# Kernel tuning notes

Hardware: AMD Instinct MI355X
Metric: run time of the kernel (lower is better)

## Reference

```python
import jax, jax.numpy as jnp
import numpy as np
from jax import lax

B, C_IN, C_OUT, H, W, K, MID = 16, 256, 256, 64, 64, 3, 64
BN_EPS = 1e-5


def setup_inputs() -> dict:
    key = jax.random.key(0)
    ks = jax.random.split(key, 16)
    inp = {
        'x': jax.random.normal(ks[0], (B, C_IN, H, W), dtype=jnp.float32),
        # 4 kernel banks: (4, c2, c1//g, k, k)
        'weight': jax.random.normal(ks[1], (4, C_OUT, C_IN, K, K), dtype=jnp.float32) * 0.05,
        'gamma': jnp.ones((C_OUT,), jnp.float32),
        'beta': jnp.zeros((C_OUT,), jnp.float32),
    }
    # four attention branches: Linear(c, mid, bias=False) -> ReLU -> Linear(mid, 4, bias=True)
    names = ['s', 'c', 'f', 'w']
    for i, n in enumerate(names):
        inp[f'fc_{n}_w1'] = jax.random.normal(ks[2 + 3 * i], (MID, C_IN), dtype=jnp.float32) * 0.05
        inp[f'fc_{n}_w2'] = jax.random.normal(ks[3 + 3 * i], (4, MID), dtype=jnp.float32) * 0.05
        inp[f'fc_{n}_b2'] = jax.random.normal(ks[4 + 3 * i], (4,), dtype=jnp.float32) * 0.05
    return inp


def _branch(pooled, w1, w2, b2):
    # pooled: [B, C]; w1: [MID, C]; w2: [4, MID]
    h = jax.nn.relu(pooled @ w1.T)
    return jax.nn.softmax(h @ w2.T + b2, axis=1)  # [B, 4]


def reference(x, weight, gamma, beta,
              fc_s_w1, fc_s_w2, fc_s_b2,
              fc_c_w1, fc_c_w2, fc_c_b2,
              fc_f_w1, fc_f_w2, fc_f_b2,
              fc_w_w1, fc_w_w2, fc_w_b2):
    b = x.shape[0]
    pooled = jnp.mean(x, axis=(2, 3))  # GAP -> [B, C]
    alpha = (_branch(pooled, fc_s_w1, fc_s_w2, fc_s_b2)
             * _branch(pooled, fc_c_w1, fc_c_w2, fc_c_b2)
             * _branch(pooled, fc_f_w1, fc_f_w2, fc_f_b2)
             * _branch(pooled, fc_w_w1, fc_w_w2, fc_w_b2))  # [B, 4]
    # per-sample dynamic kernels: [B, out_c, in_c, k, k]
    dyn_w = jnp.einsum('bn,noikl->boikl', alpha, weight)

    def conv_one(xi, wi):
        # xi: [C, H, W]; wi: [out_c, in_c, k, k]
        return lax.conv_general_dilated(
            xi[None], wi, window_strides=(1, 1), padding='SAME',
            dimension_numbers=('NCHW', 'OIHW', 'NCHW'))[0]

    out = jax.vmap(conv_one)(x, dyn_w)  # [B, out_c, H, W]

    # BatchNorm2d (training-mode batch statistics)
    mean = jnp.mean(out, axis=(0, 2, 3))
    var = jnp.var(out, axis=(0, 2, 3))
    out = (out - mean[None, :, None, None]) * jax.lax.rsqrt(var + BN_EPS)[None, :, None, None]
    return out * gamma[None, :, None, None] + beta[None, :, None, None]
```

## Files before the change

### kernel.cpp

```cpp
#include <hip/hip_runtime.h>
#include <math.h>

#define BB 16
#define CIN 256
#define COUT 256
#define HH 64
#define WW 64
#define NBANK_STRIDE 589824

typedef short bf16x8 __attribute__((ext_vector_type(8)));
typedef float f32x4 __attribute__((ext_vector_type(4)));

#define WS_XT_OFF 32768
#define WS_DW_OFF 33587200
#define WS_NEED   52461568ULL

static __device__ __forceinline__ short f2bf(float f) {
    union { float f; unsigned u; } v; v.f = f;
    unsigned r = v.u + 0x7FFF + ((v.u >> 16) & 1);
    return (short)(r >> 16);
}

struct AttnParams {
    const float* w1[4];
    const float* w2[4];
    const float* b2[4];
};

__global__ __launch_bounds__(256) void zero_kernel(float* __restrict__ ws) {
    ws[blockIdx.x * 256 + threadIdx.x] = 0.f;
}

__global__ __launch_bounds__(256) void xpose_kernel(const float* __restrict__ x,
                                                    short* __restrict__ xT,
                                                    float* __restrict__ pooled) {
    const int ci0 = blockIdx.x * 32;
    const int h = blockIdx.y;
    const int b = blockIdx.z;
    const int t = threadIdx.x;
    __shared__ __align__(16) short tile[64][40];
    {
        const int ci = t >> 3;
        const int l = t & 7;
        const float4* src = (const float4*)(x + ((size_t)(b * 256 + ci0 + ci)) * 4096 + h * 64);
        float4 v1 = src[l * 2];
        float4 v2 = src[l * 2 + 1];
        tile[l * 8 + 0][ci] = f2bf(v1.x);
        tile[l * 8 + 1][ci] = f2bf(v1.y);
        tile[l * 8 + 2][ci] = f2bf(v1.z);
        tile[l * 8 + 3][ci] = f2bf(v1.w);
        tile[l * 8 + 4][ci] = f2bf(v2.x);
        tile[l * 8 + 5][ci] = f2bf(v2.y);
        tile[l * 8 + 6][ci] = f2bf(v2.z);
        tile[l * 8 + 7][ci] = f2bf(v2.w);
        float s = v1.x + v1.y + v1.z + v1.w + v2.x + v2.y + v2.z + v2.w;
        s += __shfl_xor(s, 1, 64);
        s += __shfl_xor(s, 2, 64);
        s += __shfl_xor(s, 4, 64);
        if (l == 0) atomicAdd(&pooled[b * 256 + ci0 + ci], s);
    }
    __syncthreads();
    {
        const int w = t >> 2;
        const int s = t & 3;
        bf16x8 val = *(const bf16x8*)&tile[w][s * 8];
        *(bf16x8*)&xT[((size_t)b * 4096 + h * 64 + w) * 256 + ci0 + s * 8] = val;
    }
}

__global__ __launch_bounds__(256) void attn_kernel(AttnParams p, float* __restrict__ ws_f) {
    const int b = blockIdx.x;
    const int t = threadIdx.x;
    const int wv = t >> 6;
    const int lane = t & 63;
    __shared__ float ps[256];
    __shared__ float hs[4][64];
    __shared__ float lg[4][4];
    __shared__ float sm[4][4];
    ws_f[4096 + b * 256 + t] = 0.f;
    ps[t] = ws_f[b * 256 + t] * (1.0f / 4096.0f);
    __syncthreads();
    {
        const float4* w1v = (const float4*)(p.w1[wv] + lane * 256);
        float h = 0.f;
#pragma unroll 8
        for (int i = 0; i < 64; ++i) {
            float4 w4 = w1v[i];
            h += w4.x * ps[i * 4 + 0] + w4.y * ps[i * 4 + 1] +
                 w4.z * ps[i * 4 + 2] + w4.w * ps[i * 4 + 3];
        }
        hs[wv][lane] = fmaxf(h, 0.f);
    }
    __syncthreads();
    if (t < 16) {
        const int n = t >> 2, j = t & 3;
        const float* w2 = p.w2[n];
        float l = p.b2[n][j];
        for (int m = 0; m < 64; ++m) l += w2[j * 64 + m] * hs[n][m];
        lg[n][j] = l;
    }
    __syncthreads();
    if (t < 4) {
        const int n = t;
        float mx = fmaxf(fmaxf(lg[n][0], lg[n][1]), fmaxf(lg[n][2], lg[n][3]));
        float e0 = expf(lg[n][0] - mx), e1 = expf(lg[n][1] - mx);
        float e2 = expf(lg[n][2] - mx), e3 = expf(lg[n][3] - mx);
        float inv = 1.f / (e0 + e1 + e2 + e3);
        sm[n][0] = e0 * inv; sm[n][1] = e1 * inv; sm[n][2] = e2 * inv; sm[n][3] = e3 * inv;
    }
    __syncthreads();
    if (t < 4) ws_f[b * 256 + t] = sm[0][t] * sm[1][t] * sm[2][t] * sm[3][t];
}

__global__ __launch_bounds__(256) void dynw_kernel(const float* __restrict__ wt,
                                                   const float* __restrict__ ws_f,
                                                   short* __restrict__ dynwF) {
    const int co = blockIdx.x;
    const int ci = threadIdx.x;
    const int cotile = co >> 4;
    const int mh = co & 15;
    const int cc = ci >> 5;
    const int q = (ci >> 3) & 3;
    const int j = ci & 7;
    const int lane = q * 16 + mh;
    float w[4][9];
#pragma unroll
    for (int n = 0; n < 4; ++n) {
        const size_t base = ((size_t)(n * 256 + co) * 256 + ci) * 9;
#pragma unroll
        for (int k = 0; k < 9; ++k) w[n][k] = wt[base + k];
    }
    for (int b = 0; b < BB; ++b) {
        const float a0 = ws_f[b * 256 + 0];
        const float a1 = ws_f[b * 256 + 1];
        const float a2 = ws_f[b * 256 + 2];
        const float a3 = ws_f[b * 256 + 3];
#pragma unroll
        for (int k = 0; k < 9; ++k) {
            float v = a0 * w[0][k] + a1 * w[1][k] + a2 * w[2][k] + a3 * w[3][k];
            dynwF[(((((size_t)(b * 9 + k) * 16 + cotile) * 8 + cc) * 64 + lane) << 3) + j] = f2bf(v);
        }
    }
}

__global__ __launch_bounds__(256, 2) void conv_mfma_kernel(const short* __restrict__ xT,
                                                           const short* __restrict__ dynwF,
                                                           float* __restrict__ out,
                                                           float* __restrict__ bn_part) {
    const int id = blockIdx.x;
    const int xcd = id & 7;
    const int wi = id >> 3;
    const int b = xcd + ((wi >> 5) << 3);
    const int rem = wi & 31;
    const int mt = rem >> 4;
    const int nt = rem & 15;

    const int t = threadIdx.x;
    const int lane = t & 63;
    const int wv = t >> 6;
    const int wx = wv & 1;
    const int wy = wv >> 1;
    const int mh = lane & 15;
    const int q = lane >> 4;
    const int r0 = nt * 4;
    const int co0 = mt * 128;

    __shared__ __align__(16) short xs[396 * 64];
    __shared__ __align__(16) short As[2][4096];
    __shared__ float red[128][2][2];

    f32x4 acc[4][8];
#pragma unroll
    for (int i = 0; i < 4; ++i)
#pragma unroll
        for (int j = 0; j < 8; ++j) acc[i][j] = (f32x4){0.f, 0.f, 0.f, 0.f};

    const size_t a_b9 = (size_t)b * 9;
    const int a_ct = mt * 8 + (t >> 5);
    const int a_port16 = (t & 31) * 16;
    const int a_dst = (t >> 5) * 512 + a_port16;
    const int a_rd0 = (wy * 4) * 512 + lane * 8;

    const bf16x8 zero8 = {0, 0, 0, 0, 0, 0, 0, 0};

    for (int cc = 0; cc < 8; ++cc) {
        const int ci0 = cc * 32;
        __syncthreads();
        const short* asrc0 = dynwF + ((((a_b9 + 0) * 16 + a_ct) * 8 + cc) << 9) + a_port16;
        bf16x8 pa0 = *(const bf16x8*)(asrc0);
        bf16x8 pa1 = *(const bf16x8*)(asrc0 + 8);
#pragma unroll
        for (int i = 0; i < 7; ++i) {
            int idx = t + 256 * i;
            if (idx < 1584) {
                int p = idx >> 2;
                int sub = idx & 3;
                int lr = p / 66;
                int lc = p - lr * 66;
                int r = r0 - 1 + lr;
                int c = lc - 1;
                bf16x8 v = zero8;
                if ((unsigned)r < 64u && (unsigned)c < 64u)
                    v = *(const bf16x8*)&xT[((size_t)b * 4096 + r * 64 + c) * 256 + ci0 + sub * 8];
                *(bf16x8*)&xs[(p << 6) + ((sub ^ (p & 7)) << 3)] = v;
            }
        }
        *(bf16x8*)&As[0][a_dst] = pa0;
        *(bf16x8*)&As[0][a_dst + 8] = pa1;
        __syncthreads();
#pragma unroll
        for (int khw = 0; khw < 9; ++khw) {
            const int kh = khw / 3;
            const int kw = khw - kh * 3;
            bf16x8 na0, na1;
            if (khw < 8) {
                const short* s = dynwF + ((((a_b9 + khw + 1) * 16 + a_ct) * 8 + cc) << 9) + a_port16;
                na0 = *(const bf16x8*)(s);
                na1 = *(const bf16x8*)(s + 8);
            }
            bf16x8 bfr[8];
#pragma unroll
            for (int ni = 0; ni < 8; ++ni) {
                const int row_l = wx * 2 + (ni >> 2) + kh;
                const int col_l = (ni & 3) * 16 + kw + mh;
                const int pp = row_l * 66 + col_l;
                bfr[ni] = *(const bf16x8*)&xs[(pp << 6) + ((q ^ (pp & 7)) << 3)];
            }
#pragma unroll
            for (int mi = 0; mi < 4; ++mi) {
                bf16x8 af = *(const bf16x8*)&As[khw & 1][a_rd0 + mi * 512];
#pragma unroll
                for (int ni = 0; ni < 8; ++ni)
                    acc[mi][ni] = __builtin_amdgcn_mfma_f32_16x16x32_bf16(af, bfr[ni], acc[mi][ni], 0, 0, 0);
            }
            if (khw < 8) {
                *(bf16x8*)&As[(khw + 1) & 1][a_dst] = na0;
                *(bf16x8*)&As[(khw + 1) & 1][a_dst + 8] = na1;
                __syncthreads();
            }
        }
    }

    float s16[4][4], q16[4][4];
#pragma unroll
    for (int mi = 0; mi < 4; ++mi)
#pragma unroll
        for (int reg = 0; reg < 4; ++reg) { s16[mi][reg] = 0.f; q16[mi][reg] = 0.f; }

#pragma unroll
    for (int mi = 0; mi < 4; ++mi) {
#pragma unroll
        for (int ni = 0; ni < 8; ++ni) {
            const int pix = wx * 128 + ni * 16 + mh;
            const int h = r0 + (pix >> 6);
            const int w = pix & 63;
#pragma unroll
            for (int reg = 0; reg < 4; ++reg) {
                const int co = co0 + wy * 64 + mi * 16 + q * 4 + reg;
                const float e = acc[mi][ni][reg];
                out[(((size_t)b * 256 + co) << 12) + (h << 6) + w] = e;
                s16[mi][reg] += e;
                q16[mi][reg] += e * e;
            }
        }
    }
#pragma unroll
    for (int mi = 0; mi < 4; ++mi)
#pragma unroll
        for (int reg = 0; reg < 4; ++reg) {
            float s = s16[mi][reg], sq = q16[mi][reg];
            s += __shfl_xor(s, 1, 64);  sq += __shfl_xor(sq, 1, 64);
            s += __shfl_xor(s, 2, 64);  sq += __shfl_xor(sq, 2, 64);
            s += __shfl_xor(s, 4, 64);  sq += __shfl_xor(sq, 4, 64);
            s += __shfl_xor(s, 8, 64);  sq += __shfl_xor(sq, 8, 64);
            if (mh == 0) {
                const int co_l = wy * 64 + mi * 16 + q * 4 + reg;
                red[co_l][0][wx] = s;
                red[co_l][1][wx] = sq;
            }
        }
    __syncthreads();
    {
        const int co_l = t >> 1;
        const int st = t & 1;
        float v = red[co_l][st][0] + red[co_l][st][1];
        atomicAdd(&bn_part[(st * 256 + co0 + co_l) * 8 + (nt & 7)], v);
    }
}

__global__ __launch_bounds__(256) void bn_finalize_kernel(const float* __restrict__ bn_part,
                                                          const float* __restrict__ gamma,
                                                          const float* __restrict__ beta,
                                                          float* __restrict__ scale,
                                                          float* __restrict__ shift) {
    const int co = threadIdx.x;
    float S = 0.f, Q = 0.f;
#pragma unroll
    for (int s = 0; s < 8; ++s) {
        S += bn_part[(co) * 8 + s];
        Q += bn_part[(256 + co) * 8 + s];
    }
    const float mean = S * (1.f / 65536.f);
    const float var = Q * (1.f / 65536.f) - mean * mean;
    const float inv = rsqrtf(var + 1e-5f);
    const float sc = gamma[co] * inv;
    scale[co] = sc;
    shift[co] = beta[co] - mean * sc;
}

__global__ __launch_bounds__(256) void bn_apply_kernel(float* __restrict__ out,
                                                       const float* __restrict__ scale,
                                                       const float* __restrict__ shift) {
    const int gid = blockIdx.x * 256 + threadIdx.x;
    const int c = (gid >> 10) & 255;
    float4* p = (float4*)out;
    float4 v = p[gid];
    const float sc = scale[c], sh = shift[c];
    v.x = v.x * sc + sh;
    v.y = v.y * sc + sh;
    v.z = v.z * sc + sh;
    v.w = v.w * sc + sh;
    p[gid] = v;
}

__global__ __launch_bounds__(256) void gap_kernel(const float* __restrict__ x,
                                                  float* __restrict__ pooled) {
    const int plane = blockIdx.x;
    const float4* p = (const float4*)(x + (size_t)plane * 4096);
    const int t = threadIdx.x;
    float s = 0.f;
#pragma unroll
    for (int i = 0; i < 4; ++i) {
        float4 v = p[t + 256 * i];
        s += v.x + v.y + v.z + v.w;
    }
#pragma unroll
    for (int off = 32; off > 0; off >>= 1) s += __shfl_down(s, off, 64);
    __shared__ float red[4];
    if ((t & 63) == 0) red[t >> 6] = s;
    __syncthreads();
    if (t == 0) pooled[plane] = (red[0] + red[1] + red[2] + red[3]) * (1.0f / 4096.0f);
}

__global__ __launch_bounds__(64) void attn64_kernel(const float* __restrict__ pooled,
                                                    AttnParams p,
                                                    float* __restrict__ alpha) {
    const int b = blockIdx.x;
    const int t = threadIdx.x;
    __shared__ float ps[256];
    __shared__ float hs[64];
    __shared__ float lg[4];
    __shared__ float prod[4];
#pragma unroll
    for (int i = 0; i < 4; ++i) ps[t + 64 * i] = pooled[b * 256 + t + 64 * i];
    if (t < 4) prod[t] = 1.f;
    __syncthreads();
    for (int n = 0; n < 4; ++n) {
        const float* w1 = p.w1[n];
        float h = 0.f;
        for (int c = 0; c < 256; ++c) h += w1[t * 256 + c] * ps[c];
        hs[t] = fmaxf(h, 0.f);
        __syncthreads();
        if (t < 4) {
            const float* w2 = p.w2[n];
            float l = p.b2[n][t];
            for (int m = 0; m < 64; ++m) l += w2[t * 64 + m] * hs[m];
            lg[t] = l;
        }
        __syncthreads();
        if (t == 0) {
            float mx = fmaxf(fmaxf(lg[0], lg[1]), fmaxf(lg[2], lg[3]));
            float e0 = expf(lg[0] - mx), e1 = expf(lg[1] - mx);
            float e2 = expf(lg[2] - mx), e3 = expf(lg[3] - mx);
            float inv = 1.f / (e0 + e1 + e2 + e3);
            prod[0] *= e0 * inv; prod[1] *= e1 * inv;
            prod[2] *= e2 * inv; prod[3] *= e3 * inv;
        }
        __syncthreads();
    }
    if (t < 4) alpha[b * 4 + t] = prod[t];
}

__global__ __launch_bounds__(256) void conv_fp32_kernel(const float* __restrict__ x,
                                                        const float* __restrict__ wt,
                                                        const float* __restrict__ alpha,
                                                        float* __restrict__ out) {
    const int h = blockIdx.x;
    const int cot = blockIdx.y;
    const int b = blockIdx.z;
    const int t = threadIdx.x;
    const int tx = t & 15;
    const int ty = t >> 4;
    const int co0 = cot * 64;
    __shared__ __align__(16) float xsf[32][68];
    __shared__ __align__(16) float wshf[3][32][68];
    const float a0 = alpha[b * 4 + 0], a1 = alpha[b * 4 + 1];
    const float a2 = alpha[b * 4 + 2], a3 = alpha[b * 4 + 3];
    float acc[4][4];
#pragma unroll
    for (int i = 0; i < 4; ++i)
#pragma unroll
        for (int j = 0; j < 4; ++j) acc[i][j] = 0.f;
    const size_t xbase = (size_t)b * CIN * 4096;
    for (int kh = 0; kh < 3; ++kh) {
        const int r = h + kh - 1;
        if (r < 0 || r >= HH) continue;
        for (int chunk = 0; chunk < 8; ++chunk) {
            const int ci0 = chunk * 32;
            __syncthreads();
#pragma unroll
            for (int i = 0; i < 8; ++i) {
                int flat = t + 256 * i;
                int ci = flat >> 6;
                int w = flat & 63;
                xsf[ci][1 + w] = x[xbase + (size_t)(ci0 + ci) * 4096 + r * 64 + w];
            }
            if (t < 32) { xsf[t][0] = 0.f; xsf[t][65] = 0.f; xsf[t][66] = 0.f; xsf[t][67] = 0.f; }
#pragma unroll
            for (int j = 0; j < 24; ++j) {
                int e = t + 256 * j;
                int co = e / 96;
                int rem = e - co * 96;
                int ci = rem / 3;
                int kw = rem - ci * 3;
                size_t g = (((size_t)(co0 + co) * 256 + (ci0 + ci)) * 3 + kh) * 3 + kw;
                wshf[kw][ci][co] = a0 * wt[g] + a1 * wt[g + NBANK_STRIDE] +
                                   a2 * wt[g + 2 * NBANK_STRIDE] + a3 * wt[g + 3 * NBANK_STRIDE];
            }
            __syncthreads();
            for (int ci = 0; ci < 32; ++ci) {
                float4 w0 = *(const float4*)&wshf[0][ci][tx * 4];
                float4 w1v = *(const float4*)&wshf[1][ci][tx * 4];
                float4 w2v = *(const float4*)&wshf[2][ci][tx * 4];
                float4 xa = *(const float4*)&xsf[ci][ty * 4];
                float4 xb = *(const float4*)&xsf[ci][ty * 4 + 4];
                float v[8] = {xa.x, xa.y, xa.z, xa.w, xb.x, xb.y, xb.z, xb.w};
                float aw[3][4] = {{w0.x, w0.y, w0.z, w0.w},
                                  {w1v.x, w1v.y, w1v.z, w1v.w},
                                  {w2v.x, w2v.y, w2v.z, w2v.w}};
#pragma unroll
                for (int kw = 0; kw < 3; ++kw)
#pragma unroll
                    for (int i = 0; i < 4; ++i)
#pragma unroll
                        for (int j = 0; j < 4; ++j)
                            acc[i][j] += aw[kw][i] * v[j + kw];
            }
        }
    }
    size_t obase = (((size_t)b * COUT + co0 + tx * 4) * 64 + h) * 64 + ty * 4;
#pragma unroll
    for (int i = 0; i < 4; ++i) {
        float4 o = {acc[i][0], acc[i][1], acc[i][2], acc[i][3]};
        *(float4*)&out[obase + (size_t)i * 4096] = o;
    }
}

__global__ __launch_bounds__(256) void bn_stats_kernel(const float* __restrict__ out,
                                                       const float* __restrict__ gamma,
                                                       const float* __restrict__ beta,
                                                       float* __restrict__ scale,
                                                       float* __restrict__ shift) {
    const int co = blockIdx.x;
    const int t = threadIdx.x;
    float s = 0.f, sq = 0.f;
    for (int b = 0; b < BB; ++b) {
        const float4* p = (const float4*)(out + ((size_t)b * 256 + co) * 4096);
#pragma unroll
        for (int i = 0; i < 4; ++i) {
            float4 v = p[t + 256 * i];
            s += v.x + v.y + v.z + v.w;
            sq += v.x * v.x + v.y * v.y + v.z * v.z + v.w * v.w;
        }
    }
#pragma unroll
    for (int off = 32; off > 0; off >>= 1) {
        s += __shfl_down(s, off, 64);
        sq += __shfl_down(sq, off, 64);
    }
    __shared__ float rs[4], rq[4];
    if ((t & 63) == 0) { rs[t >> 6] = s; rq[t >> 6] = sq; }
    __syncthreads();
    if (t == 0) {
        float S = rs[0] + rs[1] + rs[2] + rs[3];
        float Q = rq[0] + rq[1] + rq[2] + rq[3];
        float mean = S * (1.f / 65536.f);
        float var = Q * (1.f / 65536.f) - mean * mean;
        float inv = rsqrtf(var + 1e-5f);
        float sc = gamma[co] * inv;
        scale[co] = sc;
        shift[co] = beta[co] - mean * sc;
    }
}

extern "C" void kernel_launch(void* const* d_in, const int* in_sizes, int n_in,
                              void* d_out, int out_size, void* d_ws, size_t ws_size,
                              hipStream_t stream) {
    (void)in_sizes; (void)n_in; (void)out_size;
    const float* x = (const float*)d_in[0];
    const float* wt = (const float*)d_in[1];
    const float* gamma = (const float*)d_in[2];
    const float* beta = (const float*)d_in[3];
    AttnParams ap;
    for (int n = 0; n < 4; ++n) {
        ap.w1[n] = (const float*)d_in[4 + 3 * n];
        ap.w2[n] = (const float*)d_in[5 + 3 * n];
        ap.b2[n] = (const float*)d_in[6 + 3 * n];
    }
    float* ws_f = (float*)d_ws;
    float* out = (float*)d_out;

    if (ws_size >= WS_NEED) {
        short* xT = (short*)((char*)d_ws + WS_XT_OFF);
        short* dynwF = (short*)((char*)d_ws + WS_DW_OFF);
        float* bn_part = ws_f + 4096;
        float* scale = ws_f;
        float* shift = ws_f + 256;

        zero_kernel<<<16, 256, 0, stream>>>(ws_f);
        xpose_kernel<<<dim3(8, 64, 16), 256, 0, stream>>>(x, xT, ws_f);
        attn_kernel<<<16, 256, 0, stream>>>(ap, ws_f);
        dynw_kernel<<<256, 256, 0, stream>>>(wt, ws_f, dynwF);
        conv_mfma_kernel<<<512, 256, 0, stream>>>(xT, dynwF, out, bn_part);
        bn_finalize_kernel<<<1, 256, 0, stream>>>(bn_part, gamma, beta, scale, shift);
        bn_apply_kernel<<<16384, 256, 0, stream>>>(out, scale, shift);
    } else {
        float* pooled = ws_f;
        float* alpha = ws_f + 4096;
        float* scale = ws_f + 4160;
        float* shift = ws_f + 4416;
        gap_kernel<<<4096, 256, 0, stream>>>(x, pooled);
        attn64_kernel<<<16, 64, 0, stream>>>(pooled, ap, alpha);
        conv_fp32_kernel<<<dim3(64, 4, 16), 256, 0, stream>>>(x, wt, alpha, out);
        bn_stats_kernel<<<256, 256, 0, stream>>>(out, gamma, beta, scale, shift);
        bn_apply_kernel<<<16384, 256, 0, stream>>>(out, scale, shift);
    }
}
```

Before: 274.3 us.

## Fuse BN finalize into apply, coalesce dynw stores, batch xpose rows, memset zeroing

Folds the BN finalize kernel into the apply kernel so each block recomputes its channel's scale and shift from the partial sums, removing one launch. The dynamic-weight kernel now stages bf16 values in shared memory and writes 16-byte vectors instead of scattered 2-byte stores. The transpose kernel handles four rows per block, accumulating the pooled sum locally so it issues fewer atomics, and the zero kernel is replaced with hipMemsetAsync. The cost is redundant per-block BN stat reads and extra barriers in the transpose and dynw kernels.

```diff
diff --git a/kernel.cpp b/kernel.cpp
--- a/kernel.cpp
+++ b/kernel.cpp
@@ -27,45 +27,46 @@
     const float* b2[4];
 };
 
-__global__ __launch_bounds__(256) void zero_kernel(float* __restrict__ ws) {
-    ws[blockIdx.x * 256 + threadIdx.x] = 0.f;
-}
-
 __global__ __launch_bounds__(256) void xpose_kernel(const float* __restrict__ x,
                                                     short* __restrict__ xT,
                                                     float* __restrict__ pooled) {
     const int ci0 = blockIdx.x * 32;
-    const int h = blockIdx.y;
+    const int h0 = blockIdx.y * 4;
     const int b = blockIdx.z;
     const int t = threadIdx.x;
     __shared__ __align__(16) short tile[64][40];
-    {
-        const int ci = t >> 3;
-        const int l = t & 7;
-        const float4* src = (const float4*)(x + ((size_t)(b * 256 + ci0 + ci)) * 4096 + h * 64);
-        float4 v1 = src[l * 2];
-        float4 v2 = src[l * 2 + 1];
-        tile[l * 8 + 0][ci] = f2bf(v1.x);
-        tile[l * 8 + 1][ci] = f2bf(v1.y);
-        tile[l * 8 + 2][ci] = f2bf(v1.z);
-        tile[l * 8 + 3][ci] = f2bf(v1.w);
-        tile[l * 8 + 4][ci] = f2bf(v2.x);
-        tile[l * 8 + 5][ci] = f2bf(v2.y);
-        tile[l * 8 + 6][ci] = f2bf(v2.z);
-        tile[l * 8 + 7][ci] = f2bf(v2.w);
-        float s = v1.x + v1.y + v1.z + v1.w + v2.x + v2.y + v2.z + v2.w;
-        s += __shfl_xor(s, 1, 64);
-        s += __shfl_xor(s, 2, 64);
-        s += __shfl_xor(s, 4, 64);
-        if (l == 0) atomicAdd(&pooled[b * 256 + ci0 + ci], s);
-    }
-    __syncthreads();
-    {
-        const int w = t >> 2;
-        const int s = t & 3;
-        bf16x8 val = *(const bf16x8*)&tile[w][s * 8];
-        *(bf16x8*)&xT[((size_t)b * 4096 + h * 64 + w) * 256 + ci0 + s * 8] = val;
-    }
+    const int ci = t >> 3;
+    const int l = t & 7;
+    const int w = t >> 2;
+    const int s4 = t & 3;
+    float sacc = 0.f;
+    for (int hh = 0; hh < 4; ++hh) {
+        const int h = h0 + hh;
+        __syncthreads();
+        {
+            const float4* src = (const float4*)(x + ((size_t)(b * 256 + ci0 + ci)) * 4096 + h * 64);
+            float4 v1 = src[l * 2];
+            float4 v2 = src[l * 2 + 1];
+            tile[l * 8 + 0][ci] = f2bf(v1.x);
+            tile[l * 8 + 1][ci] = f2bf(v1.y);
+            tile[l * 8 + 2][ci] = f2bf(v1.z);
+            tile[l * 8 + 3][ci] = f2bf(v1.w);
+            tile[l * 8 + 4][ci] = f2bf(v2.x);
+            tile[l * 8 + 5][ci] = f2bf(v2.y);
+            tile[l * 8 + 6][ci] = f2bf(v2.z);
+            tile[l * 8 + 7][ci] = f2bf(v2.w);
+            sacc += v1.x + v1.y + v1.z + v1.w + v2.x + v2.y + v2.z + v2.w;
+        }
+        __syncthreads();
+        {
+            bf16x8 val = *(const bf16x8*)&tile[w][s4 * 8];
+            *(bf16x8*)&xT[((size_t)b * 4096 + h * 64 + w) * 256 + ci0 + s4 * 8] = val;
+        }
+    }
+    sacc += __shfl_xor(sacc, 1, 64);
+    sacc += __shfl_xor(sacc, 2, 64);
+    sacc += __shfl_xor(sacc, 4, 64);
+    if (l == 0) atomicAdd(&pooled[b * 256 + ci0 + ci], sacc);
 }
 
 __global__ __launch_bounds__(256) void attn_kernel(AttnParams p, float* __restrict__ ws_f) {
@@ -119,10 +120,7 @@
     const int ci = threadIdx.x;
     const int cotile = co >> 4;
     const int mh = co & 15;
-    const int cc = ci >> 5;
-    const int q = (ci >> 3) & 3;
-    const int j = ci & 7;
-    const int lane = q * 16 + mh;
+    __shared__ __align__(16) short st[9][272];
     float w[4][9];
 #pragma unroll
     for (int n = 0; n < 4; ++n) {
@@ -136,10 +134,22 @@
         const float a2 = ws_f[b * 256 + 2];
         const float a3 = ws_f[b * 256 + 3];
 #pragma unroll
-        for (int k = 0; k < 9; ++k) {
-            float v = a0 * w[0][k] + a1 * w[1][k] + a2 * w[2][k] + a3 * w[3][k];
-            dynwF[(((((size_t)(b * 9 + k) * 16 + cotile) * 8 + cc) * 64 + lane) << 3) + j] = f2bf(v);
-        }
+        for (int k = 0; k < 9; ++k)
+            st[k][ci] = f2bf(a0 * w[0][k] + a1 * w[1][k] + a2 * w[2][k] + a3 * w[3][k]);
+        __syncthreads();
+#pragma unroll
+        for (int i = 0; i < 2; ++i) {
+            const int task = ci + 256 * i;
+            if (task < 288) {
+                const int k = task >> 5;
+                const int c5 = task & 31;
+                const int cc = c5 >> 2;
+                const int q = c5 & 3;
+                bf16x8 v = *(const bf16x8*)&st[k][cc * 32 + q * 8];
+                *(bf16x8*)&dynwF[((size_t)((b * 9 + k) * 16 + cotile) << 12) + cc * 512 + q * 128 + mh * 8] = v;
+            }
+        }
+        __syncthreads();
     }
 }
 
@@ -288,34 +298,25 @@
     }
 }
 
-__global__ __launch_bounds__(256) void bn_finalize_kernel(const float* __restrict__ bn_part,
-                                                          const float* __restrict__ gamma,
-                                                          const float* __restrict__ beta,
-                                                          float* __restrict__ scale,
-                                                          float* __restrict__ shift) {
-    const int co = threadIdx.x;
+__global__ __launch_bounds__(256) void bn_apply_kernel(float* __restrict__ out,
+                                                       const float* __restrict__ bn_part,
+                                                       const float* __restrict__ gamma,
+                                                       const float* __restrict__ beta) {
+    const int gid = blockIdx.x * 256 + threadIdx.x;
+    const int c = (blockIdx.x >> 2) & 255;
     float S = 0.f, Q = 0.f;
 #pragma unroll
     for (int s = 0; s < 8; ++s) {
-        S += bn_part[(co) * 8 + s];
-        Q += bn_part[(256 + co) * 8 + s];
+        S += bn_part[c * 8 + s];
+        Q += bn_part[(256 + c) * 8 + s];
     }
     const float mean = S * (1.f / 65536.f);
     const float var = Q * (1.f / 65536.f) - mean * mean;
     const float inv = rsqrtf(var + 1e-5f);
-    const float sc = gamma[co] * inv;
-    scale[co] = sc;
-    shift[co] = beta[co] - mean * sc;
-}
-
-__global__ __launch_bounds__(256) void bn_apply_kernel(float* __restrict__ out,
-                                                       const float* __restrict__ scale,
-                                                       const float* __restrict__ shift) {
-    const int gid = blockIdx.x * 256 + threadIdx.x;
-    const int c = (gid >> 10) & 255;
+    const float sc = gamma[c] * inv;
+    const float sh = beta[c] - mean * sc;
     float4* p = (float4*)out;
     float4 v = p[gid];
-    const float sc = scale[c], sh = shift[c];
     v.x = v.x * sc + sh;
     v.y = v.y * sc + sh;
     v.z = v.z * sc + sh;
@@ -491,6 +492,21 @@
         scale[co] = sc;
         shift[co] = beta[co] - mean * sc;
     }
+}
+
+__global__ __launch_bounds__(256) void bn_apply_sc_kernel(float* __restrict__ out,
+                                                          const float* __restrict__ scale,
+                                                          const float* __restrict__ shift) {
+    const int gid = blockIdx.x * 256 + threadIdx.x;
+    const int c = (gid >> 10) & 255;
+    float4* p = (float4*)out;
+    float4 v = p[gid];
+    const float sc = scale[c], sh = shift[c];
+    v.x = v.x * sc + sh;
+    v.y = v.y * sc + sh;
+    v.z = v.z * sc + sh;
+    v.w = v.w * sc + sh;
+    p[gid] = v;
 }
 
 extern "C" void kernel_launch(void* const* d_in, const int* in_sizes, int n_in,
@@ -514,16 +530,13 @@
         short* xT = (short*)((char*)d_ws + WS_XT_OFF);
         short* dynwF = (short*)((char*)d_ws + WS_DW_OFF);
         float* bn_part = ws_f + 4096;
-        float* scale = ws_f;
-        float* shift = ws_f + 256;
-
-        zero_kernel<<<16, 256, 0, stream>>>(ws_f);
-        xpose_kernel<<<dim3(8, 64, 16), 256, 0, stream>>>(x, xT, ws_f);
+
+        hipMemsetAsync(d_ws, 0, 32768, stream);
+        xpose_kernel<<<dim3(8, 16, 16), 256, 0, stream>>>(x, xT, ws_f);
         attn_kernel<<<16, 256, 0, stream>>>(ap, ws_f);
         dynw_kernel<<<256, 256, 0, stream>>>(wt, ws_f, dynwF);
         conv_mfma_kernel<<<512, 256, 0, stream>>>(xT, dynwF, out, bn_part);
-        bn_finalize_kernel<<<1, 256, 0, stream>>>(bn_part, gamma, beta, scale, shift);
-        bn_apply_kernel<<<16384, 256, 0, stream>>>(out, scale, shift);
+        bn_apply_kernel<<<16384, 256, 0, stream>>>(out, bn_part, gamma, beta);
     } else {
         float* pooled = ws_f;
         float* alpha = ws_f + 4096;
@@ -533,6 +546,6 @@
         attn64_kernel<<<16, 64, 0, stream>>>(pooled, ap, alpha);
         conv_fp32_kernel<<<dim3(64, 4, 16), 256, 0, stream>>>(x, wt, alpha, out);
         bn_stats_kernel<<<256, 256, 0, stream>>>(out, gamma, beta, scale, shift);
-        bn_apply_kernel<<<16384, 256, 0, stream>>>(out, scale, shift);
-    }
-}
+        bn_apply_sc_kernel<<<16384, 256, 0, stream>>>(out, scale, shift);
+    }
+}
```

After: 272.3 us. No clear change (-0.7%).
